# Kernel optimization log

Hardware: AMD Instinct MI355X
Metric: run time of the kernel (lower is better)

The kernel has to match this reference:

```python
import jax, jax.numpy as jnp
import numpy as np

B, NCOL, NCOND = 1024, 64, 64
NRODT, D, NEST, NFOREST, NHID, NCLASS = 1024, 4, 128, 100, 128, 10
EPS = 1e-5


def setup_inputs() -> dict:
    key = jax.random.key(0)
    ks = jax.random.split(key, 16)
    rng = np.random.default_rng(0)
    s = 0.1
    inp = {
        'x': jax.random.normal(ks[0], (B, NCOL), jnp.float32),
        # phi_1 numerical grouped conv: groups=NCOL, in_per_g=1, out_per_g=NCOND
        'w1': jax.random.normal(ks[1], (NCOL, 1, NCOND), jnp.float32) * s,
        'b1': jax.random.normal(ks[2], (NCOL * NCOND,), jnp.float32) * s,
        # rODTConstruction fixed permutation of the 4096 conditions
        'perm': jnp.asarray(rng.permutation(NCOND * NCOL), jnp.int32),
        'gn1_g': jnp.ones((NCOND * NCOL,), jnp.float32),
        'gn1_b': jnp.zeros((NCOND * NCOL,), jnp.float32),
        # phi_2 grouped convs: groups=NRODT, block D->D then D->1
        'w2a': jax.random.normal(ks[3], (NRODT, D, D), jnp.float32) * s,
        'b2a': jax.random.normal(ks[4], (NRODT * D,), jnp.float32) * s,
        'gn2_g': jnp.ones((NCOND * NCOL,), jnp.float32),
        'gn2_b': jnp.zeros((NCOND * NCOL,), jnp.float32),
        'w2b': jax.random.normal(ks[5], (NRODT, D, 1), jnp.float32) * s,
        'b2b': jax.random.normal(ks[6], (NRODT,), jnp.float32) * s,
        'E': jax.random.normal(ks[7], (NRODT, NHID), jnp.float32) * s,
        # eval-mode sample_without_replacement buffer: per-forest subset of rODTs
        'swr': jnp.asarray(np.argsort(rng.random((NFOREST, NRODT)), axis=-1)[:, :NEST], jnp.int32),
        'ln1_g': jnp.ones((NHID,), jnp.float32),
        'ln1_b': jnp.zeros((NHID,), jnp.float32),
        'lin1_w': jax.random.normal(ks[8], (NHID, NHID), jnp.float32) * s,
        'lin1_b': jax.random.normal(ks[9], (NHID,), jnp.float32) * s,
        'ln2_g': jnp.ones((NHID,), jnp.float32),
        'ln2_b': jnp.zeros((NHID,), jnp.float32),
        'lin2_w': jax.random.normal(ks[10], (NHID, NCLASS), jnp.float32) * s,
        'lin2_b': jax.random.normal(ks[11], (NCLASS,), jnp.float32) * s,
    }
    return inp


def _group_norm(v, g, gamma, beta):
    # v: (B, C), normalize within each of g channel groups (L=1 in the torch module)
    b, c = v.shape
    vg = v.reshape(b, g, c // g)
    mu = vg.mean(-1, keepdims=True)
    var = vg.var(-1, keepdims=True)
    vn = ((vg - mu) / jnp.sqrt(var + EPS)).reshape(b, c)
    return vn * gamma + beta


def _layer_norm(v, gamma, beta):
    mu = v.mean(-1, keepdims=True)
    var = v.var(-1, keepdims=True)
    return (v - mu) / jnp.sqrt(var + EPS) * gamma + beta


def reference(x, w1, b1, perm, gn1_g, gn1_b, w2a, b2a, gn2_g, gn2_b, w2b, b2b,
              E, swr, ln1_g, ln1_b, lin1_w, lin1_b, ln2_g, ln2_b, lin2_w, lin2_b):
    b = x.shape[0]
    # ConditionGeneration (numerical only): block-diag GEMV with in_per_group=1
    M = jax.nn.sigmoid(x[:, :, None] * w1[None, :, 0, :] + b1.reshape(NCOL, NCOND))  # (B, NCOL, NCOND)
    M = M.transpose(0, 2, 1)  # (B, NCOND, NCOL)
    # rODTConstruction: flatten + fixed permutation
    O = M.reshape(b, NCOND * NCOL)[:, perm]  # (B, 4096)
    # phi_2: GroupNorm -> grouped conv (D->D) -> ReLU -> GroupNorm -> grouped conv (D->1)
    h = _group_norm(O, NRODT, gn1_g, gn1_b).reshape(b, NRODT, D)
    h = jnp.einsum('bgi,gio->bgo', h, w2a) + b2a.reshape(NRODT, D)
    h = jax.nn.relu(h).reshape(b, NRODT * D)
    h = _group_norm(h, NRODT, gn2_g, gn2_b).reshape(b, NRODT, D)
    w = jnp.einsum('bgi,gio->bgo', h, w2b)[..., 0] + b2b  # (B, NRODT), n_head=1
    # forest construction: gather rODT subsets, softmax over estimators, weighted embed sum
    ws = jax.nn.softmax(w[:, swr], axis=-1)  # (B, NFOREST, NEST)
    Es = E[swr]  # (NFOREST, NEST, NHID)
    F = jnp.einsum('bfe,feh->bfh', ws, Es)  # (B, NFOREST, NHID)
    # phi_3 bagging MLP (eval mode: dropout = identity)
    z = _layer_norm(F, ln1_g, ln1_b)
    z = jax.nn.relu(z @ lin1_w + lin1_b)
    z = _layer_norm(z, ln2_g, ln2_b)
    y_hats = z @ lin2_w + lin2_b  # (B, NFOREST, NCLASS)
    return y_hats.mean(1)  # (B, NCLASS)
```

## Files before the change

kernel.cpp:

```cpp
#include <hip/hip_runtime.h>


#define B_      1024
#define NCOL_   64
#define NCOND_  64
#define NRODT_  1024
#define NEST_   128
#define NFOREST_ 100
#define NHID_   128
#define NCLASS_ 10
#define EPS_    1e-5f

typedef __bf16 bf16_t;
typedef bf16_t bf16x8 __attribute__((ext_vector_type(8)));
typedef float  f32x4  __attribute__((ext_vector_type(4)));

#define MFMA16(a,b,c) __builtin_amdgcn_mfma_f32_16x16x32_bf16(a,b,c,0,0,0)

#define EG_FRAGS   (NFOREST_*4*8*64)
#define W1_FRAGS   (4*8*64)
#define L2_FRAGS   (4*64)

__global__ __launch_bounds__(256) void k_prep(
    const float* __restrict__ E,     const int*   __restrict__ swr,
    const float* __restrict__ lin1w, const float* __restrict__ lin2w,
    const float* __restrict__ x,
    bf16_t* __restrict__ Eh,  bf16_t* __restrict__ El,
    bf16_t* __restrict__ Wh,  bf16_t* __restrict__ Wl,
    bf16_t* __restrict__ L2h, bf16_t* __restrict__ L2l,
    float*  __restrict__ x_t, float* __restrict__ accz)
{
    int blk = blockIdx.x, tid = threadIdx.x;
    if (blk < 800) {
        int t = blk * 256 + tid;
        int lane = t & 63, nn = (t >> 6) & 7, kk = (t >> 9) & 3, f = t >> 11;
        int q = lane >> 4, n = nn * 16 + (lane & 15);
        bf16x8 hi, lo;
#pragma unroll
        for (int j = 0; j < 8; ++j) {
            int e = kk * 32 + q * 8 + j;
            int r = swr[f * NEST_ + e];
            float v = E[r * NHID_ + n];
            bf16_t h = (bf16_t)v;
            hi[j] = h; lo[j] = (bf16_t)(v - (float)h);
        }
        *(bf16x8*)(Eh + (size_t)t * 8) = hi;
        *(bf16x8*)(El + (size_t)t * 8) = lo;
    } else if (blk < 808) {
        int t = (blk - 800) * 256 + tid;
        int lane = t & 63, nn = (t >> 6) & 7, kk = t >> 9;
        int q = lane >> 4, n = nn * 16 + (lane & 15);
        bf16x8 hi, lo;
#pragma unroll
        for (int j = 0; j < 8; ++j) {
            int k = kk * 32 + q * 8 + j;
            float v = lin1w[k * NHID_ + n];
            bf16_t h = (bf16_t)v;
            hi[j] = h; lo[j] = (bf16_t)(v - (float)h);
        }
        *(bf16x8*)(Wh + t * 8) = hi;
        *(bf16x8*)(Wl + t * 8) = lo;
    } else if (blk == 808) {
        int t = tid;
        int lane = t & 63, kk = t >> 6;
        int q = lane >> 4, n = lane & 15;
        bf16x8 hi, lo;
#pragma unroll
        for (int j = 0; j < 8; ++j) {
            int k = kk * 32 + q * 8 + j;
            float v = (n < NCLASS_) ? lin2w[k * NCLASS_ + n] : 0.f;
            bf16_t h = (bf16_t)v;
            hi[j] = h; lo[j] = (bf16_t)(v - (float)h);
        }
        *(bf16x8*)(L2h + t * 8) = hi;
        *(bf16x8*)(L2l + t * 8) = lo;
    } else if (blk < 1065) {
        int t = (blk - 809) * 256 + tid;
        x_t[t] = x[(t & 1023) * NCOL_ + (t >> 10)];
    } else {
        int t = (blk - 1065) * 256 + tid;
        if (t < B_ * NCLASS_) accz[t] = 0.f;
    }
}

__global__ __launch_bounds__(256) void k_rodt(
    const float* __restrict__ x_t,  const float* __restrict__ w1,
    const float* __restrict__ b1,   const int*  __restrict__ perm,
    const float* __restrict__ gn1g, const float* __restrict__ gn1b,
    const float* __restrict__ w2a,  const float* __restrict__ b2a,
    const float* __restrict__ gn2g, const float* __restrict__ gn2b,
    const float* __restrict__ w2b,  const float* __restrict__ b2b,
    float* __restrict__ w_t)
{
    int g  = blockIdx.x;
    int bq = threadIdx.x * 4;

    int4 p4 = ((const int4*)perm)[g];
    int col[4]  = { p4.x & 63, p4.y & 63, p4.z & 63, p4.w & 63 };
    int cond[4] = { p4.x >> 6, p4.y >> 6, p4.z >> 6, p4.w >> 6 };
    float w1v[4], b1v[4];
#pragma unroll
    for (int j = 0; j < 4; ++j) {
        w1v[j] = w1[col[j] * NCOND_ + cond[j]];
        b1v[j] = b1[col[j] * NCOND_ + cond[j]];
    }
    float4 g1  = ((const float4*)gn1g)[g];
    float4 o1  = ((const float4*)gn1b)[g];
    float4 ba  = ((const float4*)b2a)[g];
    float4 g2  = ((const float4*)gn2g)[g];
    float4 o2  = ((const float4*)gn2b)[g];
    float4 wb4 = ((const float4*)w2b)[g];
    float  bb  = b2b[g];
    float4 wa[4];
    const float4* w2a4 = (const float4*)w2a;
#pragma unroll
    for (int i = 0; i < 4; ++i) wa[i] = w2a4[g * 4 + i];

    float xv[4][4];
#pragma unroll
    for (int j = 0; j < 4; ++j) {
        float4 t = *(const float4*)&x_t[col[j] * B_ + bq];
        xv[j][0] = t.x; xv[j][1] = t.y; xv[j][2] = t.z; xv[j][3] = t.w;
    }

    float outv[4];
#pragma unroll
    for (int bi = 0; bi < 4; ++bi) {
        float v[4];
#pragma unroll
        for (int j = 0; j < 4; ++j) {
            float t = xv[j][bi] * w1v[j] + b1v[j];
            v[j] = 1.0f / (1.0f + __expf(-t));
        }
        float mu = (v[0] + v[1] + v[2] + v[3]) * 0.25f;
        float var = 0.f;
#pragma unroll
        for (int j = 0; j < 4; ++j) { float d = v[j] - mu; var += d * d; }
        var *= 0.25f;
        float rs = rsqrtf(var + EPS_);
        float h[4];
        h[0] = (v[0] - mu) * rs * g1.x + o1.x;
        h[1] = (v[1] - mu) * rs * g1.y + o1.y;
        h[2] = (v[2] - mu) * rs * g1.z + o1.z;
        h[3] = (v[3] - mu) * rs * g1.w + o1.w;

        float4 a = ba;
#pragma unroll
        for (int i = 0; i < 4; ++i) {
            a.x += h[i] * wa[i].x; a.y += h[i] * wa[i].y;
            a.z += h[i] * wa[i].z; a.w += h[i] * wa[i].w;
        }
        float t2[4];
        t2[0] = fmaxf(a.x, 0.f); t2[1] = fmaxf(a.y, 0.f);
        t2[2] = fmaxf(a.z, 0.f); t2[3] = fmaxf(a.w, 0.f);

        float mu2 = (t2[0] + t2[1] + t2[2] + t2[3]) * 0.25f;
        float var2 = 0.f;
#pragma unroll
        for (int j = 0; j < 4; ++j) { float d = t2[j] - mu2; var2 += d * d; }
        var2 *= 0.25f;
        float rs2 = rsqrtf(var2 + EPS_);

        float wvv = bb;
        wvv += ((t2[0] - mu2) * rs2 * g2.x + o2.x) * wb4.x;
        wvv += ((t2[1] - mu2) * rs2 * g2.y + o2.y) * wb4.y;
        wvv += ((t2[2] - mu2) * rs2 * g2.z + o2.z) * wb4.z;
        wvv += ((t2[3] - mu2) * rs2 * g2.w + o2.w) * wb4.w;
        outv[bi] = wvv;
    }
    *(float4*)&w_t[(size_t)g * B_ + bq] = make_float4(outv[0], outv[1], outv[2], outv[3]);
}

__global__ __launch_bounds__(256, 4) void k_forest(
    const float*  __restrict__ w_t, const int* __restrict__ swr,
    const bf16_t* __restrict__ Eh,  const bf16_t* __restrict__ El,
    const bf16_t* __restrict__ Wh,  const bf16_t* __restrict__ Wl,
    const bf16_t* __restrict__ L2h, const bf16_t* __restrict__ L2l,
    const float* __restrict__ ln1g, const float* __restrict__ ln1b,
    const float* __restrict__ lin1b,
    const float* __restrict__ ln2g, const float* __restrict__ ln2b,
    float* __restrict__ acc)
{
    __shared__ float zsh[4][16 * 132];

    int tid  = threadIdx.x;
    int wid  = tid >> 6;
    int lane = tid & 63;
    int q    = lane >> 4;
    int mc   = lane & 15;

    int n    = blockIdx.x;
    int swiz = (n & 7) * 200 + (n >> 3);
    int f    = swiz >> 4;
    int bt   = swiz & 15;
    int b0   = bt * 64 + wid * 16;

    const int* swrf = swr + f * NEST_;
    float* zw = zsh[wid];

    float ex[4][8];
    float mx = -1e30f;
#pragma unroll
    for (int kk = 0; kk < 4; ++kk) {
        int4 r0 = *(const int4*)(swrf + kk * 32 + q * 8);
        int4 r1 = *(const int4*)(swrf + kk * 32 + q * 8 + 4);
        int rr[8] = { r0.x, r0.y, r0.z, r0.w, r1.x, r1.y, r1.z, r1.w };
#pragma unroll
        for (int j = 0; j < 8; ++j) {
            float v = w_t[rr[j] * B_ + b0 + mc];
            ex[kk][j] = v;
            mx = fmaxf(mx, v);
        }
    }
    mx = fmaxf(mx, __shfl_xor(mx, 16));
    mx = fmaxf(mx, __shfl_xor(mx, 32));
    float s = 0.f;
#pragma unroll
    for (int kk = 0; kk < 4; ++kk)
#pragma unroll
        for (int j = 0; j < 8; ++j) { ex[kk][j] = __expf(ex[kk][j] - mx); s += ex[kk][j]; }
    s += __shfl_xor(s, 16);
    s += __shfl_xor(s, 32);
    float inv = 1.f / s;

    bf16x8 afr[4];
#pragma unroll
    for (int kk = 0; kk < 4; ++kk)
#pragma unroll
        for (int j = 0; j < 8; ++j) afr[kk][j] = (bf16_t)(ex[kk][j] * inv);

    f32x4 accF[8];
#pragma unroll
    for (int nn = 0; nn < 8; ++nn) accF[nn] = (f32x4){0.f, 0.f, 0.f, 0.f};
    const bf16x8* EHf = (const bf16x8*)Eh;
    const bf16x8* ELf = (const bf16x8*)El;
#pragma unroll
    for (int kk = 0; kk < 4; ++kk) {
        size_t bi = (size_t)(f * 4 + kk) * 8;
#pragma unroll
        for (int nn = 0; nn < 8; ++nn) {
            bf16x8 bh = EHf[(bi + nn) * 64 + lane];
            bf16x8 bl = ELf[(bi + nn) * 64 + lane];
            accF[nn] = MFMA16(afr[kk], bh, accF[nn]);
            accF[nn] = MFMA16(afr[kk], bl, accF[nn]);
        }
    }

    float mu[4], rs[4];
#pragma unroll
    for (int reg = 0; reg < 4; ++reg) {
        float ps = 0.f, pq = 0.f;
#pragma unroll
        for (int nn = 0; nn < 8; ++nn) { float v = accF[nn][reg]; ps += v; pq += v * v; }
#pragma unroll
        for (int o = 1; o <= 8; o <<= 1) { ps += __shfl_xor(ps, o); pq += __shfl_xor(pq, o); }
        float m_ = ps * (1.f / NHID_);
        mu[reg] = m_;
        rs[reg] = rsqrtf(pq * (1.f / NHID_) - m_ * m_ + EPS_);
    }
    {
#pragma unroll
        for (int nn = 0; nn < 8; ++nn) {
            int c = nn * 16 + mc;
            float gv = ln1g[c], bv = ln1b[c];
#pragma unroll
            for (int reg = 0; reg < 4; ++reg)
                zw[(q * 4 + reg) * 132 + c] = (accF[nn][reg] - mu[reg]) * rs[reg] * gv + bv;
        }
    }

    bf16x8 a2[4];
#pragma unroll
    for (int kk = 0; kk < 4; ++kk) {
        int dwb = kk * 32 + q * 8;
        f32x4 u0 = *(const f32x4*)&zw[mc * 132 + dwb];
        f32x4 u1 = *(const f32x4*)&zw[mc * 132 + dwb + 4];
#pragma unroll
        for (int j = 0; j < 4; ++j) { a2[kk][j] = (bf16_t)u0[j]; a2[kk][4 + j] = (bf16_t)u1[j]; }
    }
    f32x4 accA[8];
#pragma unroll
    for (int nn = 0; nn < 8; ++nn) accA[nn] = (f32x4){0.f, 0.f, 0.f, 0.f};
    const bf16x8* WHf = (const bf16x8*)Wh;
    const bf16x8* WLf = (const bf16x8*)Wl;
#pragma unroll
    for (int kk = 0; kk < 4; ++kk) {
#pragma unroll
        for (int nn = 0; nn < 8; ++nn) {
            bf16x8 bh = WHf[(kk * 8 + nn) * 64 + lane];
            bf16x8 bl = WLf[(kk * 8 + nn) * 64 + lane];
            accA[nn] = MFMA16(a2[kk], bh, accA[nn]);
            accA[nn] = MFMA16(a2[kk], bl, accA[nn]);
        }
    }

#pragma unroll
    for (int nn = 0; nn < 8; ++nn) {
        float bv = lin1b[nn * 16 + mc];
#pragma unroll
        for (int reg = 0; reg < 4; ++reg)
            accA[nn][reg] = fmaxf(accA[nn][reg] + bv, 0.f);
    }
    float mu2[4], rs2[4];
#pragma unroll
    for (int reg = 0; reg < 4; ++reg) {
        float ps = 0.f, pq = 0.f;
#pragma unroll
        for (int nn = 0; nn < 8; ++nn) { float v = accA[nn][reg]; ps += v; pq += v * v; }
#pragma unroll
        for (int o = 1; o <= 8; o <<= 1) { ps += __shfl_xor(ps, o); pq += __shfl_xor(pq, o); }
        float m_ = ps * (1.f / NHID_);
        mu2[reg] = m_;
        rs2[reg] = rsqrtf(pq * (1.f / NHID_) - m_ * m_ + EPS_);
    }
    {
#pragma unroll
        for (int nn = 0; nn < 8; ++nn) {
            int c = nn * 16 + mc;
            float gv = ln2g[c], bv = ln2b[c];
#pragma unroll
            for (int reg = 0; reg < 4; ++reg)
                zw[(q * 4 + reg) * 132 + c] = (accA[nn][reg] - mu2[reg]) * rs2[reg] * gv + bv;
        }
    }

    f32x4 accO = {0.f, 0.f, 0.f, 0.f};
    const bf16x8* LHf = (const bf16x8*)L2h;
    const bf16x8* LLf = (const bf16x8*)L2l;
#pragma unroll
    for (int kk = 0; kk < 4; ++kk) {
        int dwb = kk * 32 + q * 8;
        f32x4 u0 = *(const f32x4*)&zw[mc * 132 + dwb];
        f32x4 u1 = *(const f32x4*)&zw[mc * 132 + dwb + 4];
        bf16x8 a3;
#pragma unroll
        for (int j = 0; j < 4; ++j) { a3[j] = (bf16_t)u0[j]; a3[4 + j] = (bf16_t)u1[j]; }
        accO = MFMA16(a3, LHf[kk * 64 + lane], accO);
        accO = MFMA16(a3, LLf[kk * 64 + lane], accO);
    }
    if (mc < NCLASS_) {
#pragma unroll
        for (int reg = 0; reg < 4; ++reg)
            atomicAdd(&acc[(b0 + q * 4 + reg) * NCLASS_ + mc], accO[reg]);
    }
}

__global__ __launch_bounds__(256) void k_final(
    const float* __restrict__ acc, const float* __restrict__ lin2b,
    float* __restrict__ out)
{
    int i = blockIdx.x * 256 + threadIdx.x;
    if (i < B_ * NCLASS_) {
        int c = i % NCLASS_;
        out[i] = acc[i] * (1.f / NFOREST_) + lin2b[c];
    }
}

extern "C" void kernel_launch(void* const* d_in, const int* in_sizes, int n_in,
                              void* d_out, int out_size, void* d_ws, size_t ws_size,
                              hipStream_t stream)
{
    const float* x     = (const float*)d_in[0];
    const float* w1    = (const float*)d_in[1];
    const float* b1    = (const float*)d_in[2];
    const int*   perm  = (const int*)  d_in[3];
    const float* gn1g  = (const float*)d_in[4];
    const float* gn1b  = (const float*)d_in[5];
    const float* w2a   = (const float*)d_in[6];
    const float* b2a   = (const float*)d_in[7];
    const float* gn2g  = (const float*)d_in[8];
    const float* gn2b  = (const float*)d_in[9];
    const float* w2b   = (const float*)d_in[10];
    const float* b2b   = (const float*)d_in[11];
    const float* E     = (const float*)d_in[12];
    const int*   swr   = (const int*)  d_in[13];
    const float* ln1g  = (const float*)d_in[14];
    const float* ln1b  = (const float*)d_in[15];
    const float* lin1w = (const float*)d_in[16];
    const float* lin1b = (const float*)d_in[17];
    const float* ln2g  = (const float*)d_in[18];
    const float* ln2b  = (const float*)d_in[19];
    const float* lin2w = (const float*)d_in[20];
    const float* lin2b = (const float*)d_in[21];

    char* base = (char*)d_ws;
    float*  w_t  = (float*)base;
    float*  accp = (float*)(base + 4u * 1024 * 1024);
    float*  x_t  = (float*)(base + 4u * 1024 * 1024 + 64 * 1024);
    bf16_t* Eh   = (bf16_t*)(base + 4u * 1024 * 1024 + 64 * 1024 + 256 * 1024);
    bf16_t* El   = Eh  + (size_t)EG_FRAGS * 8;
    bf16_t* Wh   = El  + (size_t)EG_FRAGS * 8;
    bf16_t* Wl   = Wh  + (size_t)W1_FRAGS * 8;
    bf16_t* L2h  = Wl  + (size_t)W1_FRAGS * 8;
    bf16_t* L2l  = L2h + (size_t)L2_FRAGS * 8;

    k_prep<<<1105, 256, 0, stream>>>(E, swr, lin1w, lin2w, x,
                                     Eh, El, Wh, Wl, L2h, L2l, x_t, accp);

    k_rodt<<<NRODT_, 256, 0, stream>>>(
        x_t, w1, b1, perm, gn1g, gn1b, w2a, b2a, gn2g, gn2b, w2b, b2b, w_t);

    k_forest<<<NFOREST_ * 16, 256, 0, stream>>>(
        w_t, swr, Eh, El, Wh, Wl, L2h, L2l,
        ln1g, ln1b, lin1b, ln2g, ln2b, accp);

    k_final<<<(B_ * NCLASS_ + 255) / 256, 256, 0, stream>>>(
        accp, lin2b, (float*)d_out);
}
```

Before: 148.9 us.

## Fuse rODT stage into prep kernel and stage forest activations as bf16

Moves the per-rODT phi_2 computation into the prep kernel as extra blocks. The separate x transpose and the k_rodt launch go away, and x is read directly with strided accesses instead. In k_forest, the LDS staging buffer now holds bf16 instead of float, so the A fragments are loaded as one bf16x8 vector without per-element conversion. That halves shared memory use, and the launch bound is raised to 8 blocks per CU. The trade-offs are uncoalesced reads of x and possible register pressure under the higher occupancy target.

```diff
diff --git a/kernel.cpp b/kernel.cpp
--- a/kernel.cpp
+++ b/kernel.cpp
@@ -21,14 +21,21 @@
 #define W1_FRAGS   (4*8*64)
 #define L2_FRAGS   (4*64)
 
+#define ZLD 136
+
 __global__ __launch_bounds__(256) void k_prep(
     const float* __restrict__ E,     const int*   __restrict__ swr,
     const float* __restrict__ lin1w, const float* __restrict__ lin2w,
-    const float* __restrict__ x,
+    const float* __restrict__ x,     const float* __restrict__ w1,
+    const float* __restrict__ b1,    const int*   __restrict__ perm,
+    const float* __restrict__ gn1g,  const float* __restrict__ gn1b,
+    const float* __restrict__ w2a,   const float* __restrict__ b2a,
+    const float* __restrict__ gn2g,  const float* __restrict__ gn2b,
+    const float* __restrict__ w2b,   const float* __restrict__ b2b,
     bf16_t* __restrict__ Eh,  bf16_t* __restrict__ El,
     bf16_t* __restrict__ Wh,  bf16_t* __restrict__ Wl,
     bf16_t* __restrict__ L2h, bf16_t* __restrict__ L2l,
-    float*  __restrict__ x_t, float* __restrict__ accz)
+    float*  __restrict__ accz, float* __restrict__ w_t)
 {
     int blk = blockIdx.x, tid = threadIdx.x;
     if (blk < 800) {
@@ -74,104 +81,91 @@
         }
         *(bf16x8*)(L2h + t * 8) = hi;
         *(bf16x8*)(L2l + t * 8) = lo;
-    } else if (blk < 1065) {
+    } else if (blk < 849) {
         int t = (blk - 809) * 256 + tid;
-        x_t[t] = x[(t & 1023) * NCOL_ + (t >> 10)];
+        if (t < B_ * NCLASS_) accz[t] = 0.f;
     } else {
-        int t = (blk - 1065) * 256 + tid;
-        if (t < B_ * NCLASS_) accz[t] = 0.f;
+        int g  = blk - 849;
+        int bq = tid * 4;
+
+        int4 p4 = ((const int4*)perm)[g];
+        int col[4]  = { p4.x & 63, p4.y & 63, p4.z & 63, p4.w & 63 };
+        int cond[4] = { p4.x >> 6, p4.y >> 6, p4.z >> 6, p4.w >> 6 };
+        float w1v[4], b1v[4];
+#pragma unroll
+        for (int j = 0; j < 4; ++j) {
+            w1v[j] = w1[col[j] * NCOND_ + cond[j]];
+            b1v[j] = b1[col[j] * NCOND_ + cond[j]];
+        }
+        float4 g1  = ((const float4*)gn1g)[g];
+        float4 o1  = ((const float4*)gn1b)[g];
+        float4 ba  = ((const float4*)b2a)[g];
+        float4 g2  = ((const float4*)gn2g)[g];
+        float4 o2  = ((const float4*)gn2b)[g];
+        float4 wb4 = ((const float4*)w2b)[g];
+        float  bb  = b2b[g];
+        float4 wa[4];
+        const float4* w2a4 = (const float4*)w2a;
+#pragma unroll
+        for (int i = 0; i < 4; ++i) wa[i] = w2a4[g * 4 + i];
+
+        float xv[4][4];
+#pragma unroll
+        for (int bi = 0; bi < 4; ++bi)
+#pragma unroll
+            for (int j = 0; j < 4; ++j)
+                xv[j][bi] = x[(size_t)(bq + bi) * NCOL_ + col[j]];
+
+        float outv[4];
+#pragma unroll
+        for (int bi = 0; bi < 4; ++bi) {
+            float v[4];
+#pragma unroll
+            for (int j = 0; j < 4; ++j) {
+                float t = xv[j][bi] * w1v[j] + b1v[j];
+                v[j] = 1.0f / (1.0f + __expf(-t));
+            }
+            float mu = (v[0] + v[1] + v[2] + v[3]) * 0.25f;
+            float var = 0.f;
+#pragma unroll
+            for (int j = 0; j < 4; ++j) { float d = v[j] - mu; var += d * d; }
+            var *= 0.25f;
+            float rs = rsqrtf(var + EPS_);
+            float h[4];
+            h[0] = (v[0] - mu) * rs * g1.x + o1.x;
+            h[1] = (v[1] - mu) * rs * g1.y + o1.y;
+            h[2] = (v[2] - mu) * rs * g1.z + o1.z;
+            h[3] = (v[3] - mu) * rs * g1.w + o1.w;
+
+            float4 a = ba;
+#pragma unroll
+            for (int i = 0; i < 4; ++i) {
+                a.x += h[i] * wa[i].x; a.y += h[i] * wa[i].y;
+                a.z += h[i] * wa[i].z; a.w += h[i] * wa[i].w;
+            }
+            float t2[4];
+            t2[0] = fmaxf(a.x, 0.f); t2[1] = fmaxf(a.y, 0.f);
+            t2[2] = fmaxf(a.z, 0.f); t2[3] = fmaxf(a.w, 0.f);
+
+            float mu2 = (t2[0] + t2[1] + t2[2] + t2[3]) * 0.25f;
+            float var2 = 0.f;
+#pragma unroll
+            for (int j = 0; j < 4; ++j) { float d = t2[j] - mu2; var2 += d * d; }
+            var2 *= 0.25f;
+            float rs2 = rsqrtf(var2 + EPS_);
+
+            float wvv = bb;
+            wvv += ((t2[0] - mu2) * rs2 * g2.x + o2.x) * wb4.x;
+            wvv += ((t2[1] - mu2) * rs2 * g2.y + o2.y) * wb4.y;
+            wvv += ((t2[2] - mu2) * rs2 * g2.z + o2.z) * wb4.z;
+            wvv += ((t2[3] - mu2) * rs2 * g2.w + o2.w) * wb4.w;
+            outv[bi] = wvv;
+        }
+        *(float4*)&w_t[(size_t)g * B_ + bq] = make_float4(outv[0], outv[1], outv[2], outv[3]);
     }
 }
 
-__global__ __launch_bounds__(256) void k_rodt(
-    const float* __restrict__ x_t,  const float* __restrict__ w1,
-    const float* __restrict__ b1,   const int*  __restrict__ perm,
-    const float* __restrict__ gn1g, const float* __restrict__ gn1b,
-    const float* __restrict__ w2a,  const float* __restrict__ b2a,
-    const float* __restrict__ gn2g, const float* __restrict__ gn2b,
-    const float* __restrict__ w2b,  const float* __restrict__ b2b,
-    float* __restrict__ w_t)
-{
-    int g  = blockIdx.x;
-    int bq = threadIdx.x * 4;
-
-    int4 p4 = ((const int4*)perm)[g];
-    int col[4]  = { p4.x & 63, p4.y & 63, p4.z & 63, p4.w & 63 };
-    int cond[4] = { p4.x >> 6, p4.y >> 6, p4.z >> 6, p4.w >> 6 };
-    float w1v[4], b1v[4];
-#pragma unroll
-    for (int j = 0; j < 4; ++j) {
-        w1v[j] = w1[col[j] * NCOND_ + cond[j]];
-        b1v[j] = b1[col[j] * NCOND_ + cond[j]];
-    }
-    float4 g1  = ((const float4*)gn1g)[g];
-    float4 o1  = ((const float4*)gn1b)[g];
-    float4 ba  = ((const float4*)b2a)[g];
-    float4 g2  = ((const float4*)gn2g)[g];
-    float4 o2  = ((const float4*)gn2b)[g];
-    float4 wb4 = ((const float4*)w2b)[g];
-    float  bb  = b2b[g];
-    float4 wa[4];
-    const float4* w2a4 = (const float4*)w2a;
-#pragma unroll
-    for (int i = 0; i < 4; ++i) wa[i] = w2a4[g * 4 + i];
-
-    float xv[4][4];
-#pragma unroll
-    for (int j = 0; j < 4; ++j) {
-        float4 t = *(const float4*)&x_t[col[j] * B_ + bq];
-        xv[j][0] = t.x; xv[j][1] = t.y; xv[j][2] = t.z; xv[j][3] = t.w;
-    }
-
-    float outv[4];
-#pragma unroll
-    for (int bi = 0; bi < 4; ++bi) {
-        float v[4];
-#pragma unroll
-        for (int j = 0; j < 4; ++j) {
-            float t = xv[j][bi] * w1v[j] + b1v[j];
-            v[j] = 1.0f / (1.0f + __expf(-t));
-        }
-        float mu = (v[0] + v[1] + v[2] + v[3]) * 0.25f;
-        float var = 0.f;
-#pragma unroll
-        for (int j = 0; j < 4; ++j) { float d = v[j] - mu; var += d * d; }
-        var *= 0.25f;
-        float rs = rsqrtf(var + EPS_);
-        float h[4];
-        h[0] = (v[0] - mu) * rs * g1.x + o1.x;
-        h[1] = (v[1] - mu) * rs * g1.y + o1.y;
-        h[2] = (v[2] - mu) * rs * g1.z + o1.z;
-        h[3] = (v[3] - mu) * rs * g1.w + o1.w;
-
-        float4 a = ba;
-#pragma unroll
-        for (int i = 0; i < 4; ++i) {
-            a.x += h[i] * wa[i].x; a.y += h[i] * wa[i].y;
-            a.z += h[i] * wa[i].z; a.w += h[i] * wa[i].w;
-        }
-        float t2[4];
-        t2[0] = fmaxf(a.x, 0.f); t2[1] = fmaxf(a.y, 0.f);
-        t2[2] = fmaxf(a.z, 0.f); t2[3] = fmaxf(a.w, 0.f);
-
-        float mu2 = (t2[0] + t2[1] + t2[2] + t2[3]) * 0.25f;
-        float var2 = 0.f;
-#pragma unroll
-        for (int j = 0; j < 4; ++j) { float d = t2[j] - mu2; var2 += d * d; }
-        var2 *= 0.25f;
-        float rs2 = rsqrtf(var2 + EPS_);
-
-        float wvv = bb;
-        wvv += ((t2[0] - mu2) * rs2 * g2.x + o2.x) * wb4.x;
-        wvv += ((t2[1] - mu2) * rs2 * g2.y + o2.y) * wb4.y;
-        wvv += ((t2[2] - mu2) * rs2 * g2.z + o2.z) * wb4.z;
-        wvv += ((t2[3] - mu2) * rs2 * g2.w + o2.w) * wb4.w;
-        outv[bi] = wvv;
-    }
-    *(float4*)&w_t[(size_t)g * B_ + bq] = make_float4(outv[0], outv[1], outv[2], outv[3]);
-}
-
-__global__ __launch_bounds__(256, 4) void k_forest(
+__global__ __launch_bounds__(256, 8) void k_forest(
     const float*  __restrict__ w_t, const int* __restrict__ swr,
     const bf16_t* __restrict__ Eh,  const bf16_t* __restrict__ El,
     const bf16_t* __restrict__ Wh,  const bf16_t* __restrict__ Wl,
@@ -181,7 +175,7 @@
     const float* __restrict__ ln2g, const float* __restrict__ ln2b,
     float* __restrict__ acc)
 {
-    __shared__ float zsh[4][16 * 132];
+    __shared__ __align__(16) bf16_t zsh[4][16 * ZLD];
 
     int tid  = threadIdx.x;
     int wid  = tid >> 6;
@@ -196,7 +190,7 @@
     int b0   = bt * 64 + wid * 16;
 
     const int* swrf = swr + f * NEST_;
-    float* zw = zsh[wid];
+    bf16_t* zw = zsh[wid];
 
     float ex[4][8];
     float mx = -1e30f;
@@ -265,19 +259,16 @@
             float gv = ln1g[c], bv = ln1b[c];
 #pragma unroll
             for (int reg = 0; reg < 4; ++reg)
-                zw[(q * 4 + reg) * 132 + c] = (accF[nn][reg] - mu[reg]) * rs[reg] * gv + bv;
+                zw[(q * 4 + reg) * ZLD + c] =
+                    (bf16_t)((accF[nn][reg] - mu[reg]) * rs[reg] * gv + bv);
         }
     }
 
     bf16x8 a2[4];
 #pragma unroll
-    for (int kk = 0; kk < 4; ++kk) {
-        int dwb = kk * 32 + q * 8;
-        f32x4 u0 = *(const f32x4*)&zw[mc * 132 + dwb];
-        f32x4 u1 = *(const f32x4*)&zw[mc * 132 + dwb + 4];
-#pragma unroll
-        for (int j = 0; j < 4; ++j) { a2[kk][j] = (bf16_t)u0[j]; a2[kk][4 + j] = (bf16_t)u1[j]; }
-    }
+    for (int kk = 0; kk < 4; ++kk)
+        a2[kk] = *(const bf16x8*)&zw[mc * ZLD + kk * 32 + q * 8];
+
     f32x4 accA[8];
 #pragma unroll
     for (int nn = 0; nn < 8; ++nn) accA[nn] = (f32x4){0.f, 0.f, 0.f, 0.f};
@@ -320,7 +311,8 @@
             float gv = ln2g[c], bv = ln2b[c];
 #pragma unroll
             for (int reg = 0; reg < 4; ++reg)
-                zw[(q * 4 + reg) * 132 + c] = (accA[nn][reg] - mu2[reg]) * rs2[reg] * gv + bv;
+                zw[(q * 4 + reg) * ZLD + c] =
+                    (bf16_t)((accA[nn][reg] - mu2[reg]) * rs2[reg] * gv + bv);
         }
     }
 
@@ -329,12 +321,7 @@
     const bf16x8* LLf = (const bf16x8*)L2l;
 #pragma unroll
     for (int kk = 0; kk < 4; ++kk) {
-        int dwb = kk * 32 + q * 8;
-        f32x4 u0 = *(const f32x4*)&zw[mc * 132 + dwb];
-        f32x4 u1 = *(const f32x4*)&zw[mc * 132 + dwb + 4];
-        bf16x8 a3;
-#pragma unroll
-        for (int j = 0; j < 4; ++j) { a3[j] = (bf16_t)u0[j]; a3[4 + j] = (bf16_t)u1[j]; }
+        bf16x8 a3 = *(const bf16x8*)&zw[mc * ZLD + kk * 32 + q * 8];
         accO = MFMA16(a3, LHf[kk * 64 + lane], accO);
         accO = MFMA16(a3, LLf[kk * 64 + lane], accO);
     }
@@ -386,7 +373,6 @@
     char* base = (char*)d_ws;
     float*  w_t  = (float*)base;
     float*  accp = (float*)(base + 4u * 1024 * 1024);
-    float*  x_t  = (float*)(base + 4u * 1024 * 1024 + 64 * 1024);
     bf16_t* Eh   = (bf16_t*)(base + 4u * 1024 * 1024 + 64 * 1024 + 256 * 1024);
     bf16_t* El   = Eh  + (size_t)EG_FRAGS * 8;
     bf16_t* Wh   = El  + (size_t)EG_FRAGS * 8;
@@ -394,11 +380,9 @@
     bf16_t* L2h  = Wl  + (size_t)W1_FRAGS * 8;
     bf16_t* L2l  = L2h + (size_t)L2_FRAGS * 8;
 
-    k_prep<<<1105, 256, 0, stream>>>(E, swr, lin1w, lin2w, x,
-                                     Eh, El, Wh, Wl, L2h, L2l, x_t, accp);
-
-    k_rodt<<<NRODT_, 256, 0, stream>>>(
-        x_t, w1, b1, perm, gn1g, gn1b, w2a, b2a, gn2g, gn2b, w2b, b2b, w_t);
+    k_prep<<<1873, 256, 0, stream>>>(
+        E, swr, lin1w, lin2w, x, w1, b1, perm, gn1g, gn1b, w2a, b2a,
+        gn2g, gn2b, w2b, b2b, Eh, El, Wh, Wl, L2h, L2l, accp, w_t);
 
     k_forest<<<NFOREST_ * 16, 256, 0, stream>>>(
         w_t, swr, Eh, El, Wh, Wl, L2h, L2l,
```

Result: slower. 187.0 us (+25.6%).

## Process two 16-row batch tiles per wave in forest kernel to reuse B fragments

Applied to the files above, without the earlier changes.

Each wave in k_forest now handles 32 batch rows, as two 16-row MFMA tiles, instead of 16. Every loaded E, lin1 and lin2 bf16 fragment therefore feeds two MFMAs, which halves global fragment traffic per output, and the grid shrinks from 1600 to 800 blocks. The LDS staging buffer also becomes bf16 with a 136 stride, so A-fragments are read with one vector load and no fp32-to-bf16 conversion on the read side. In exchange, register pressure roughly doubles (launch bounds lowered to 3 waves per SIMD), and there are fewer blocks to hide latency.

```diff
diff --git a/kernel.cpp b/kernel.cpp
--- a/kernel.cpp
+++ b/kernel.cpp
@@ -20,6 +20,8 @@
 #define EG_FRAGS   (NFOREST_*4*8*64)
 #define W1_FRAGS   (4*8*64)
 #define L2_FRAGS   (4*64)
+
+#define ZLD 136
 
 __global__ __launch_bounds__(256) void k_prep(
     const float* __restrict__ E,     const int*   __restrict__ swr,
@@ -171,7 +173,7 @@
     *(float4*)&w_t[(size_t)g * B_ + bq] = make_float4(outv[0], outv[1], outv[2], outv[3]);
 }
 
-__global__ __launch_bounds__(256, 4) void k_forest(
+__global__ __launch_bounds__(256, 3) void k_forest(
     const float*  __restrict__ w_t, const int* __restrict__ swr,
     const bf16_t* __restrict__ Eh,  const bf16_t* __restrict__ El,
     const bf16_t* __restrict__ Wh,  const bf16_t* __restrict__ Wl,
@@ -181,7 +183,7 @@
     const float* __restrict__ ln2g, const float* __restrict__ ln2b,
     float* __restrict__ acc)
 {
-    __shared__ float zsh[4][16 * 132];
+    __shared__ __align__(16) bf16_t zsh[4][32 * ZLD];
 
     int tid  = threadIdx.x;
     int wid  = tid >> 6;
@@ -190,16 +192,16 @@
     int mc   = lane & 15;
 
     int n    = blockIdx.x;
-    int swiz = (n & 7) * 200 + (n >> 3);
-    int f    = swiz >> 4;
-    int bt   = swiz & 15;
-    int b0   = bt * 64 + wid * 16;
+    int swiz = (n & 7) * 100 + (n >> 3);
+    int f    = swiz >> 3;
+    int bt   = swiz & 7;
+    int b0   = bt * 128 + wid * 32;
 
     const int* swrf = swr + f * NEST_;
-    float* zw = zsh[wid];
-
-    float ex[4][8];
-    float mx = -1e30f;
+    bf16_t* zw = zsh[wid];
+
+    float ex[2][4][8];
+    float mx0 = -1e30f, mx1 = -1e30f;
 #pragma unroll
     for (int kk = 0; kk < 4; ++kk) {
         int4 r0 = *(const int4*)(swrf + kk * 32 + q * 8);
@@ -207,31 +209,41 @@
         int rr[8] = { r0.x, r0.y, r0.z, r0.w, r1.x, r1.y, r1.z, r1.w };
 #pragma unroll
         for (int j = 0; j < 8; ++j) {
-            float v = w_t[rr[j] * B_ + b0 + mc];
-            ex[kk][j] = v;
-            mx = fmaxf(mx, v);
-        }
-    }
-    mx = fmaxf(mx, __shfl_xor(mx, 16));
-    mx = fmaxf(mx, __shfl_xor(mx, 32));
-    float s = 0.f;
+            const float* wp = w_t + (size_t)rr[j] * B_ + b0 + mc;
+            float v0 = wp[0];
+            float v1 = wp[16];
+            ex[0][kk][j] = v0; mx0 = fmaxf(mx0, v0);
+            ex[1][kk][j] = v1; mx1 = fmaxf(mx1, v1);
+        }
+    }
+    mx0 = fmaxf(mx0, __shfl_xor(mx0, 16)); mx0 = fmaxf(mx0, __shfl_xor(mx0, 32));
+    mx1 = fmaxf(mx1, __shfl_xor(mx1, 16)); mx1 = fmaxf(mx1, __shfl_xor(mx1, 32));
+    float s0 = 0.f, s1 = 0.f;
 #pragma unroll
     for (int kk = 0; kk < 4; ++kk)
 #pragma unroll
-        for (int j = 0; j < 8; ++j) { ex[kk][j] = __expf(ex[kk][j] - mx); s += ex[kk][j]; }
-    s += __shfl_xor(s, 16);
-    s += __shfl_xor(s, 32);
-    float inv = 1.f / s;
-
-    bf16x8 afr[4];
+        for (int j = 0; j < 8; ++j) {
+            ex[0][kk][j] = __expf(ex[0][kk][j] - mx0); s0 += ex[0][kk][j];
+            ex[1][kk][j] = __expf(ex[1][kk][j] - mx1); s1 += ex[1][kk][j];
+        }
+    s0 += __shfl_xor(s0, 16); s0 += __shfl_xor(s0, 32);
+    s1 += __shfl_xor(s1, 16); s1 += __shfl_xor(s1, 32);
+    float inv0 = 1.f / s0, inv1 = 1.f / s1;
+
+    bf16x8 afr[2][4];
 #pragma unroll
     for (int kk = 0; kk < 4; ++kk)
 #pragma unroll
-        for (int j = 0; j < 8; ++j) afr[kk][j] = (bf16_t)(ex[kk][j] * inv);
-
-    f32x4 accF[8];
-#pragma unroll
-    for (int nn = 0; nn < 8; ++nn) accF[nn] = (f32x4){0.f, 0.f, 0.f, 0.f};
+        for (int j = 0; j < 8; ++j) {
+            afr[0][kk][j] = (bf16_t)(ex[0][kk][j] * inv0);
+            afr[1][kk][j] = (bf16_t)(ex[1][kk][j] * inv1);
+        }
+
+    f32x4 accF[2][8];
+#pragma unroll
+    for (int t = 0; t < 2; ++t)
+#pragma unroll
+        for (int nn = 0; nn < 8; ++nn) accF[t][nn] = (f32x4){0.f, 0.f, 0.f, 0.f};
     const bf16x8* EHf = (const bf16x8*)Eh;
     const bf16x8* ELf = (const bf16x8*)El;
 #pragma unroll
@@ -241,46 +253,51 @@
         for (int nn = 0; nn < 8; ++nn) {
             bf16x8 bh = EHf[(bi + nn) * 64 + lane];
             bf16x8 bl = ELf[(bi + nn) * 64 + lane];
-            accF[nn] = MFMA16(afr[kk], bh, accF[nn]);
-            accF[nn] = MFMA16(afr[kk], bl, accF[nn]);
-        }
-    }
-
-    float mu[4], rs[4];
-#pragma unroll
-    for (int reg = 0; reg < 4; ++reg) {
-        float ps = 0.f, pq = 0.f;
-#pragma unroll
-        for (int nn = 0; nn < 8; ++nn) { float v = accF[nn][reg]; ps += v; pq += v * v; }
-#pragma unroll
-        for (int o = 1; o <= 8; o <<= 1) { ps += __shfl_xor(ps, o); pq += __shfl_xor(pq, o); }
-        float m_ = ps * (1.f / NHID_);
-        mu[reg] = m_;
-        rs[reg] = rsqrtf(pq * (1.f / NHID_) - m_ * m_ + EPS_);
-    }
-    {
-#pragma unroll
-        for (int nn = 0; nn < 8; ++nn) {
-            int c = nn * 16 + mc;
-            float gv = ln1g[c], bv = ln1b[c];
+            accF[0][nn] = MFMA16(afr[0][kk], bh, accF[0][nn]);
+            accF[1][nn] = MFMA16(afr[1][kk], bh, accF[1][nn]);
+            accF[0][nn] = MFMA16(afr[0][kk], bl, accF[0][nn]);
+            accF[1][nn] = MFMA16(afr[1][kk], bl, accF[1][nn]);
+        }
+    }
+
+    float mu[2][4], rs[2][4];
+#pragma unroll
+    for (int t = 0; t < 2; ++t)
+#pragma unroll
+        for (int reg = 0; reg < 4; ++reg) {
+            float ps = 0.f, pq = 0.f;
+#pragma unroll
+            for (int nn = 0; nn < 8; ++nn) { float v = accF[t][nn][reg]; ps += v; pq += v * v; }
+#pragma unroll
+            for (int o = 1; o <= 8; o <<= 1) { ps += __shfl_xor(ps, o); pq += __shfl_xor(pq, o); }
+            float m_ = ps * (1.f / NHID_);
+            mu[t][reg] = m_;
+            rs[t][reg] = rsqrtf(pq * (1.f / NHID_) - m_ * m_ + EPS_);
+        }
+#pragma unroll
+    for (int nn = 0; nn < 8; ++nn) {
+        int c = nn * 16 + mc;
+        float gv = ln1g[c], bv = ln1b[c];
+#pragma unroll
+        for (int t = 0; t < 2; ++t)
 #pragma unroll
             for (int reg = 0; reg < 4; ++reg)
-                zw[(q * 4 + reg) * 132 + c] = (accF[nn][reg] - mu[reg]) * rs[reg] * gv + bv;
-        }
-    }
-
-    bf16x8 a2[4];
-#pragma unroll
-    for (int kk = 0; kk < 4; ++kk) {
-        int dwb = kk * 32 + q * 8;
-        f32x4 u0 = *(const f32x4*)&zw[mc * 132 + dwb];
-        f32x4 u1 = *(const f32x4*)&zw[mc * 132 + dwb + 4];
-#pragma unroll
-        for (int j = 0; j < 4; ++j) { a2[kk][j] = (bf16_t)u0[j]; a2[kk][4 + j] = (bf16_t)u1[j]; }
-    }
-    f32x4 accA[8];
-#pragma unroll
-    for (int nn = 0; nn < 8; ++nn) accA[nn] = (f32x4){0.f, 0.f, 0.f, 0.f};
+                zw[(t * 16 + q * 4 + reg) * ZLD + c] =
+                    (bf16_t)((accF[t][nn][reg] - mu[t][reg]) * rs[t][reg] * gv + bv);
+    }
+
+    bf16x8 a2[2][4];
+#pragma unroll
+    for (int t = 0; t < 2; ++t)
+#pragma unroll
+        for (int kk = 0; kk < 4; ++kk)
+            a2[t][kk] = *(const bf16x8*)&zw[(t * 16 + mc) * ZLD + kk * 32 + q * 8];
+
+    f32x4 accA[2][8];
+#pragma unroll
+    for (int t = 0; t < 2; ++t)
+#pragma unroll
+        for (int nn = 0; nn < 8; ++nn) accA[t][nn] = (f32x4){0.f, 0.f, 0.f, 0.f};
     const bf16x8* WHf = (const bf16x8*)Wh;
     const bf16x8* WLf = (const bf16x8*)Wl;
 #pragma unroll
@@ -289,8 +306,10 @@
         for (int nn = 0; nn < 8; ++nn) {
             bf16x8 bh = WHf[(kk * 8 + nn) * 64 + lane];
             bf16x8 bl = WLf[(kk * 8 + nn) * 64 + lane];
-            accA[nn] = MFMA16(a2[kk], bh, accA[nn]);
-            accA[nn] = MFMA16(a2[kk], bl, accA[nn]);
+            accA[0][nn] = MFMA16(a2[0][kk], bh, accA[0][nn]);
+            accA[1][nn] = MFMA16(a2[1][kk], bh, accA[1][nn]);
+            accA[0][nn] = MFMA16(a2[0][kk], bl, accA[0][nn]);
+            accA[1][nn] = MFMA16(a2[1][kk], bl, accA[1][nn]);
         }
     }
 
@@ -298,50 +317,57 @@
     for (int nn = 0; nn < 8; ++nn) {
         float bv = lin1b[nn * 16 + mc];
 #pragma unroll
-        for (int reg = 0; reg < 4; ++reg)
-            accA[nn][reg] = fmaxf(accA[nn][reg] + bv, 0.f);
-    }
-    float mu2[4], rs2[4];
-#pragma unroll
-    for (int reg = 0; reg < 4; ++reg) {
-        float ps = 0.f, pq = 0.f;
-#pragma unroll
-        for (int nn = 0; nn < 8; ++nn) { float v = accA[nn][reg]; ps += v; pq += v * v; }
-#pragma unroll
-        for (int o = 1; o <= 8; o <<= 1) { ps += __shfl_xor(ps, o); pq += __shfl_xor(pq, o); }
-        float m_ = ps * (1.f / NHID_);
-        mu2[reg] = m_;
-        rs2[reg] = rsqrtf(pq * (1.f / NHID_) - m_ * m_ + EPS_);
-    }
-    {
-#pragma unroll
-        for (int nn = 0; nn < 8; ++nn) {
-            int c = nn * 16 + mc;
-            float gv = ln2g[c], bv = ln2b[c];
+        for (int t = 0; t < 2; ++t)
 #pragma unroll
             for (int reg = 0; reg < 4; ++reg)
-                zw[(q * 4 + reg) * 132 + c] = (accA[nn][reg] - mu2[reg]) * rs2[reg] * gv + bv;
-        }
-    }
-
-    f32x4 accO = {0.f, 0.f, 0.f, 0.f};
+                accA[t][nn][reg] = fmaxf(accA[t][nn][reg] + bv, 0.f);
+    }
+    float mu2[2][4], rs2[2][4];
+#pragma unroll
+    for (int t = 0; t < 2; ++t)
+#pragma unroll
+        for (int reg = 0; reg < 4; ++reg) {
+            float ps = 0.f, pq = 0.f;
+#pragma unroll
+            for (int nn = 0; nn < 8; ++nn) { float v = accA[t][nn][reg]; ps += v; pq += v * v; }
+#pragma unroll
+            for (int o = 1; o <= 8; o <<= 1) { ps += __shfl_xor(ps, o); pq += __shfl_xor(pq, o); }
+            float m_ = ps * (1.f / NHID_);
+            mu2[t][reg] = m_;
+            rs2[t][reg] = rsqrtf(pq * (1.f / NHID_) - m_ * m_ + EPS_);
+        }
+#pragma unroll
+    for (int nn = 0; nn < 8; ++nn) {
+        int c = nn * 16 + mc;
+        float gv = ln2g[c], bv = ln2b[c];
+#pragma unroll
+        for (int t = 0; t < 2; ++t)
+#pragma unroll
+            for (int reg = 0; reg < 4; ++reg)
+                zw[(t * 16 + q * 4 + reg) * ZLD + c] =
+                    (bf16_t)((accA[t][nn][reg] - mu2[t][reg]) * rs2[t][reg] * gv + bv);
+    }
+
+    f32x4 accO[2] = { (f32x4){0.f,0.f,0.f,0.f}, (f32x4){0.f,0.f,0.f,0.f} };
     const bf16x8* LHf = (const bf16x8*)L2h;
     const bf16x8* LLf = (const bf16x8*)L2l;
 #pragma unroll
     for (int kk = 0; kk < 4; ++kk) {
-        int dwb = kk * 32 + q * 8;
-        f32x4 u0 = *(const f32x4*)&zw[mc * 132 + dwb];
-        f32x4 u1 = *(const f32x4*)&zw[mc * 132 + dwb + 4];
-        bf16x8 a3;
-#pragma unroll
-        for (int j = 0; j < 4; ++j) { a3[j] = (bf16_t)u0[j]; a3[4 + j] = (bf16_t)u1[j]; }
-        accO = MFMA16(a3, LHf[kk * 64 + lane], accO);
-        accO = MFMA16(a3, LLf[kk * 64 + lane], accO);
+        bf16x8 lh = LHf[kk * 64 + lane];
+        bf16x8 ll = LLf[kk * 64 + lane];
+#pragma unroll
+        for (int t = 0; t < 2; ++t) {
+            bf16x8 a3 = *(const bf16x8*)&zw[(t * 16 + mc) * ZLD + kk * 32 + q * 8];
+            accO[t] = MFMA16(a3, lh, accO[t]);
+            accO[t] = MFMA16(a3, ll, accO[t]);
+        }
     }
     if (mc < NCLASS_) {
 #pragma unroll
-        for (int reg = 0; reg < 4; ++reg)
-            atomicAdd(&acc[(b0 + q * 4 + reg) * NCLASS_ + mc], accO[reg]);
+        for (int t = 0; t < 2; ++t)
+#pragma unroll
+            for (int reg = 0; reg < 4; ++reg)
+                atomicAdd(&acc[(b0 + t * 16 + q * 4 + reg) * NCLASS_ + mc], accO[t][reg]);
     }
 }
 
@@ -400,7 +426,7 @@
     k_rodt<<<NRODT_, 256, 0, stream>>>(
         x_t, w1, b1, perm, gn1g, gn1b, w2a, b2a, gn2g, gn2b, w2b, b2b, w_t);
 
-    k_forest<<<NFOREST_ * 16, 256, 0, stream>>>(
+    k_forest<<<NFOREST_ * 8, 256, 0, stream>>>(
         w_t, swr, Eh, El, Wh, Wl, L2h, L2l,
         ln1g, ln1b, lin1b, ln2g, ln2b, accp);
 
```

Result: slower. 178.6 us (+20.0%).

## Stage forest E and lin1 weight fragments in LDS via async global-to-LDS loads

Applied to the files above, without the earlier changes.

k_forest now uses 512-thread blocks that each cover 128 batch rows instead of 64. At block start it copies the per-forest E hi/lo fragments and the lin1 hi/lo fragments into 128 KB of LDS using global_load_lds, so the loads overlap the softmax, and the MFMA loops then read operands from LDS rather than global memory. Intermediate layer-norm outputs are stored as bf16 with a padded stride in reused LDS, and lin2 fragments are also staged into LDS. This halves global weight traffic per batch row. The 128 KB of LDS per block limits occupancy to one block per CU, and the added __syncthreads barriers serialize the phases.

```diff
diff --git a/kernel.cpp b/kernel.cpp
--- a/kernel.cpp
+++ b/kernel.cpp
@@ -20,6 +20,13 @@
 #define EG_FRAGS   (NFOREST_*4*8*64)
 #define W1_FRAGS   (4*8*64)
 #define L2_FRAGS   (4*64)
+
+#define ZLD 136
+
+#define GLDS16(gp, lp) \
+    __builtin_amdgcn_global_load_lds( \
+        (const __attribute__((address_space(1))) unsigned int*)(gp), \
+        (__attribute__((address_space(3))) unsigned int*)(lp), 16, 0, 0)
 
 __global__ __launch_bounds__(256) void k_prep(
     const float* __restrict__ E,     const int*   __restrict__ swr,
@@ -171,7 +178,7 @@
     *(float4*)&w_t[(size_t)g * B_ + bq] = make_float4(outv[0], outv[1], outv[2], outv[3]);
 }
 
-__global__ __launch_bounds__(256, 4) void k_forest(
+__global__ __launch_bounds__(512, 2) void k_forest(
     const float*  __restrict__ w_t, const int* __restrict__ swr,
     const bf16_t* __restrict__ Eh,  const bf16_t* __restrict__ El,
     const bf16_t* __restrict__ Wh,  const bf16_t* __restrict__ Wl,
@@ -181,7 +188,8 @@
     const float* __restrict__ ln2g, const float* __restrict__ ln2b,
     float* __restrict__ acc)
 {
-    __shared__ float zsh[4][16 * 132];
+    __shared__ __align__(16) char bufE[65536];
+    __shared__ __align__(16) char bufW[65536];
 
     int tid  = threadIdx.x;
     int wid  = tid >> 6;
@@ -190,13 +198,27 @@
     int mc   = lane & 15;
 
     int n    = blockIdx.x;
-    int swiz = (n & 7) * 200 + (n >> 3);
-    int f    = swiz >> 4;
-    int bt   = swiz & 15;
-    int b0   = bt * 64 + wid * 16;
+    int lin  = (n & 7) * 100 + (n >> 3);
+    int f    = lin >> 3;
+    int bt   = lin & 7;
+    int b0   = bt * 128 + wid * 16;
 
     const int* swrf = swr + f * NEST_;
-    float* zw = zsh[wid];
+
+    {
+        const char* Ehp = (const char*)Eh + (size_t)f * 32 * 1024;
+        const char* Elp = (const char*)El + (size_t)f * 32 * 1024;
+        const char* Whp = (const char*)Wh;
+        const char* Wlp = (const char*)Wl;
+#pragma unroll
+        for (int c = 0; c < 4; ++c) {
+            int r = wid * 4 + c;
+            GLDS16(Ehp + r * 1024 + lane * 16, bufE + r * 1024);
+            GLDS16(Elp + r * 1024 + lane * 16, bufE + 32768 + r * 1024);
+            GLDS16(Whp + r * 1024 + lane * 16, bufW + r * 1024);
+            GLDS16(Wlp + r * 1024 + lane * 16, bufW + 32768 + r * 1024);
+        }
+    }
 
     float ex[4][8];
     float mx = -1e30f;
@@ -229,18 +251,18 @@
 #pragma unroll
         for (int j = 0; j < 8; ++j) afr[kk][j] = (bf16_t)(ex[kk][j] * inv);
 
+    __syncthreads();
+
     f32x4 accF[8];
 #pragma unroll
     for (int nn = 0; nn < 8; ++nn) accF[nn] = (f32x4){0.f, 0.f, 0.f, 0.f};
-    const bf16x8* EHf = (const bf16x8*)Eh;
-    const bf16x8* ELf = (const bf16x8*)El;
 #pragma unroll
     for (int kk = 0; kk < 4; ++kk) {
-        size_t bi = (size_t)(f * 4 + kk) * 8;
 #pragma unroll
         for (int nn = 0; nn < 8; ++nn) {
-            bf16x8 bh = EHf[(bi + nn) * 64 + lane];
-            bf16x8 bl = ELf[(bi + nn) * 64 + lane];
+            int r = kk * 8 + nn;
+            bf16x8 bh = *(const bf16x8*)(bufE + r * 1024 + lane * 16);
+            bf16x8 bl = *(const bf16x8*)(bufE + 32768 + r * 1024 + lane * 16);
             accF[nn] = MFMA16(afr[kk], bh, accF[nn]);
             accF[nn] = MFMA16(afr[kk], bl, accF[nn]);
         }
@@ -258,37 +280,44 @@
         mu[reg] = m_;
         rs[reg] = rsqrtf(pq * (1.f / NHID_) - m_ * m_ + EPS_);
     }
+
+    __syncthreads();
+
     {
+        const char* src = (wid < 4) ? ((const char*)L2h + wid * 1024)
+                                    : ((const char*)L2l + (wid - 4) * 1024);
+        char* dst = bufE + 40960 + ((wid < 4) ? wid * 1024
+                                              : 4096 + (wid - 4) * 1024);
+        GLDS16(src + lane * 16, dst);
+    }
+
+    bf16_t* zw = (bf16_t*)bufE + wid * (16 * ZLD);
+
+#pragma unroll
+    for (int nn = 0; nn < 8; ++nn) {
+        int c = nn * 16 + mc;
+        float gv = ln1g[c], bv = ln1b[c];
+#pragma unroll
+        for (int reg = 0; reg < 4; ++reg)
+            zw[(q * 4 + reg) * ZLD + c] =
+                (bf16_t)((accF[nn][reg] - mu[reg]) * rs[reg] * gv + bv);
+    }
+
+    bf16x8 a2[4];
+#pragma unroll
+    for (int kk = 0; kk < 4; ++kk)
+        a2[kk] = *(const bf16x8*)&zw[mc * ZLD + kk * 32 + q * 8];
+
+    f32x4 accA[8];
+#pragma unroll
+    for (int nn = 0; nn < 8; ++nn) accA[nn] = (f32x4){0.f, 0.f, 0.f, 0.f};
+#pragma unroll
+    for (int kk = 0; kk < 4; ++kk) {
 #pragma unroll
         for (int nn = 0; nn < 8; ++nn) {
-            int c = nn * 16 + mc;
-            float gv = ln1g[c], bv = ln1b[c];
-#pragma unroll
-            for (int reg = 0; reg < 4; ++reg)
-                zw[(q * 4 + reg) * 132 + c] = (accF[nn][reg] - mu[reg]) * rs[reg] * gv + bv;
-        }
-    }
-
-    bf16x8 a2[4];
-#pragma unroll
-    for (int kk = 0; kk < 4; ++kk) {
-        int dwb = kk * 32 + q * 8;
-        f32x4 u0 = *(const f32x4*)&zw[mc * 132 + dwb];
-        f32x4 u1 = *(const f32x4*)&zw[mc * 132 + dwb + 4];
-#pragma unroll
-        for (int j = 0; j < 4; ++j) { a2[kk][j] = (bf16_t)u0[j]; a2[kk][4 + j] = (bf16_t)u1[j]; }
-    }
-    f32x4 accA[8];
-#pragma unroll
-    for (int nn = 0; nn < 8; ++nn) accA[nn] = (f32x4){0.f, 0.f, 0.f, 0.f};
-    const bf16x8* WHf = (const bf16x8*)Wh;
-    const bf16x8* WLf = (const bf16x8*)Wl;
-#pragma unroll
-    for (int kk = 0; kk < 4; ++kk) {
-#pragma unroll
-        for (int nn = 0; nn < 8; ++nn) {
-            bf16x8 bh = WHf[(kk * 8 + nn) * 64 + lane];
-            bf16x8 bl = WLf[(kk * 8 + nn) * 64 + lane];
+            int r = kk * 8 + nn;
+            bf16x8 bh = *(const bf16x8*)(bufW + r * 1024 + lane * 16);
+            bf16x8 bl = *(const bf16x8*)(bufW + 32768 + r * 1024 + lane * 16);
             accA[nn] = MFMA16(a2[kk], bh, accA[nn]);
             accA[nn] = MFMA16(a2[kk], bl, accA[nn]);
         }
@@ -313,30 +342,26 @@
         mu2[reg] = m_;
         rs2[reg] = rsqrtf(pq * (1.f / NHID_) - m_ * m_ + EPS_);
     }
-    {
-#pragma unroll
-        for (int nn = 0; nn < 8; ++nn) {
-            int c = nn * 16 + mc;
-            float gv = ln2g[c], bv = ln2b[c];
-#pragma unroll
-            for (int reg = 0; reg < 4; ++reg)
-                zw[(q * 4 + reg) * 132 + c] = (accA[nn][reg] - mu2[reg]) * rs2[reg] * gv + bv;
-        }
-    }
+#pragma unroll
+    for (int nn = 0; nn < 8; ++nn) {
+        int c = nn * 16 + mc;
+        float gv = ln2g[c], bv = ln2b[c];
+#pragma unroll
+        for (int reg = 0; reg < 4; ++reg)
+            zw[(q * 4 + reg) * ZLD + c] =
+                (bf16_t)((accA[nn][reg] - mu2[reg]) * rs2[reg] * gv + bv);
+    }
+
+    __syncthreads();
 
     f32x4 accO = {0.f, 0.f, 0.f, 0.f};
-    const bf16x8* LHf = (const bf16x8*)L2h;
-    const bf16x8* LLf = (const bf16x8*)L2l;
 #pragma unroll
     for (int kk = 0; kk < 4; ++kk) {
-        int dwb = kk * 32 + q * 8;
-        f32x4 u0 = *(const f32x4*)&zw[mc * 132 + dwb];
-        f32x4 u1 = *(const f32x4*)&zw[mc * 132 + dwb + 4];
-        bf16x8 a3;
-#pragma unroll
-        for (int j = 0; j < 4; ++j) { a3[j] = (bf16_t)u0[j]; a3[4 + j] = (bf16_t)u1[j]; }
-        accO = MFMA16(a3, LHf[kk * 64 + lane], accO);
-        accO = MFMA16(a3, LLf[kk * 64 + lane], accO);
+        bf16x8 a3 = *(const bf16x8*)&zw[mc * ZLD + kk * 32 + q * 8];
+        bf16x8 lh = *(const bf16x8*)(bufE + 40960 + kk * 1024 + lane * 16);
+        bf16x8 ll = *(const bf16x8*)(bufE + 40960 + 4096 + kk * 1024 + lane * 16);
+        accO = MFMA16(a3, lh, accO);
+        accO = MFMA16(a3, ll, accO);
     }
     if (mc < NCLASS_) {
 #pragma unroll
@@ -400,7 +425,7 @@
     k_rodt<<<NRODT_, 256, 0, stream>>>(
         x_t, w1, b1, perm, gn1g, gn1b, w2a, b2a, gn2g, gn2b, w2b, b2b, w_t);
 
-    k_forest<<<NFOREST_ * 16, 256, 0, stream>>>(
+    k_forest<<<NFOREST_ * 8, 512, 0, stream>>>(
         w_t, swr, Eh, El, Wh, Wl, L2h, L2l,
         ln1g, ln1b, lin1b, ln2g, ln2b, accp);
 
```

Result: slower. 158.9 us (+6.7%).
